# Kernel optimization log

Measured on AMD Instinct MI355X. Metric: run time of the kernel, lower is better.

The kernel has to match this reference:

```python
import jax, jax.numpy as jnp
import numpy as np

B, C, H, Wd, IN_CAPS = 128, 32, 12, 12, 8
OUT_CH, OUT_CAPS, ROUTING_ITERS = 10, 16, 3


def setup_inputs() -> dict:
    key = jax.random.key(0)
    k1, k2 = jax.random.split(key)
    x = jax.random.normal(k1, (B, C, H, Wd, IN_CAPS), dtype=jnp.float32)
    W = jax.random.normal(k2, (1, 1, C, OUT_CH, OUT_CAPS, IN_CAPS), dtype=jnp.float32)
    return {"x": x, "W": W}


def _squash(s):
    # s: [..., out_caps]
    sn = jnp.sum(s * s, axis=-1, keepdims=True)
    return sn * s / ((1.0 + sn) * jnp.sqrt(sn))


def reference(x, W):
    b = x.shape[0]
    # [B, H, W, C, in_caps]
    u = jnp.transpose(x, (0, 2, 3, 1, 4))
    Wm = W[0, 0]  # [C, out_ch, out_caps, in_caps]
    # u_hat[b,h,w,c,o,p] = sum_q Wm[c,o,p,q] * u[b,h,w,c,q]
    u_hat = jnp.einsum('copq,bhwcq->bhwcop', Wm, u)
    u_hat = u_hat.reshape(b, -1, OUT_CH, OUT_CAPS)  # [B, N, O, P]

    b_ij = jnp.zeros(u_hat.shape[:-1], dtype=u_hat.dtype)  # [B, N, O]
    v_j = None
    for i in range(ROUTING_ITERS):
        c_ij = jax.nn.softmax(b_ij, axis=-1)[..., None]  # [B, N, O, 1]
        s_j = jnp.sum(c_ij * u_hat, axis=1)              # [B, O, P]
        v_j = _squash(s_j)                               # [B, O, P]
        if i < ROUTING_ITERS - 1:
            a_j = jnp.sum(u_hat * v_j[:, None], axis=-1)  # [B, N, O]
            b_ij = b_ij + a_j
    return v_j
```

## Files before the change

### kernel.cpp

```cpp
#include <hip/hip_runtime.h>


#define BB 128
#define CC 32
#define HWN 144
#define QQ 8
#define OO 10
#define PP 16

__global__ __launch_bounds__(256, 1)
void digitcaps_routing(const float* __restrict__ x, const float* __restrict__ Wm,
                       float* __restrict__ out) {
    const int b    = blockIdx.x;
    const int tid  = threadIdx.x;
    const int c    = tid >> 3;
    const int slot = tid & 7;

    __shared__ float usum_s[CC * QQ];
    __shared__ float Wv_s[CC * OO * QQ];
    __shared__ float t_s[CC * OO * QQ];
    __shared__ float v_s[OO * PP];

    const float* xb = x + (size_t)b * (CC * HWN * QQ);
    const float* xc = xb + c * (HWN * QQ);

    float us[QQ];
#pragma unroll
    for (int q = 0; q < QQ; ++q) us[q] = 0.f;
#pragma unroll
    for (int i = 0; i < 18; ++i) {
        const int hw = slot + (i << 3);
        const float4* p4 = (const float4*)(xc + hw * QQ);
        float4 a = p4[0], d = p4[1];
        us[0] += a.x; us[1] += a.y; us[2] += a.z; us[3] += a.w;
        us[4] += d.x; us[5] += d.y; us[6] += d.z; us[7] += d.w;
    }
#pragma unroll
    for (int m = 1; m <= 4; m <<= 1) {
#pragma unroll
        for (int q = 0; q < QQ; ++q) us[q] += __shfl_xor(us[q], m);
    }
    if (slot == 0) {
#pragma unroll
        for (int q = 0; q < QQ; ++q) usum_s[c * QQ + q] = us[q];
    }
    __syncthreads();

    if (tid < OO * PP) {
        const int o = tid >> 4, p = tid & 15;
        float s = 0.f;
        for (int cc = 0; cc < CC; ++cc) {
            const float4* w4 = (const float4*)(Wm + (((cc * OO + o) * PP + p) * QQ));
            float4 w0 = w4[0], w1 = w4[1];
            const float* u0 = &usum_s[cc * QQ];
            s += w0.x * u0[0] + w0.y * u0[1] + w0.z * u0[2] + w0.w * u0[3]
               + w1.x * u0[4] + w1.y * u0[5] + w1.z * u0[6] + w1.w * u0[7];
        }
        s *= 0.1f;
        float sn = s * s;
#pragma unroll
        for (int m = 1; m <= 8; m <<= 1) sn += __shfl_xor(sn, m);
        const float fac = sqrtf(sn) / (1.f + sn);
        v_s[tid] = s * fac;
    }
    for (int k = tid; k < CC * OO * QQ; k += 256) Wv_s[k] = 0.f;
    __syncthreads();

    for (int iter = 0; iter < 2; ++iter) {
        for (int k = tid; k < CC * OO * QQ; k += 256) {
            const int cc  = k / (OO * QQ);
            const int rem = k - cc * (OO * QQ);
            const int o   = rem >> 3, q = rem & 7;
            const float* wp = Wm + ((cc * OO + o) * PP) * QQ + q;
            float acc = 0.f;
#pragma unroll
            for (int p = 0; p < PP; ++p) acc += wp[p * QQ] * v_s[o * PP + p];
            Wv_s[k] += acc;
        }
        __syncthreads();

        float wv[OO][QQ];
#pragma unroll
        for (int o = 0; o < OO; ++o)
#pragma unroll
            for (int q = 0; q < QQ; ++q) wv[o][q] = Wv_s[(c * OO + o) * QQ + q];

        float tl[OO][QQ];
#pragma unroll
        for (int o = 0; o < OO; ++o)
#pragma unroll
            for (int q = 0; q < QQ; ++q) tl[o][q] = 0.f;

        for (int i = 0; i < 18; ++i) {
            const int hw = slot + (i << 3);
            const float4* p4 = (const float4*)(xc + hw * QQ);
            float4 a = p4[0], d = p4[1];
            float u[QQ] = {a.x, a.y, a.z, a.w, d.x, d.y, d.z, d.w};
            float lg[OO];
            float mx = -1e30f;
#pragma unroll
            for (int o = 0; o < OO; ++o) {
                float t = 0.f;
#pragma unroll
                for (int q = 0; q < QQ; ++q) t += u[q] * wv[o][q];
                lg[o] = t;
                mx = fmaxf(mx, t);
            }
            float ssum = 0.f;
#pragma unroll
            for (int o = 0; o < OO; ++o) { lg[o] = __expf(lg[o] - mx); ssum += lg[o]; }
            const float inv = 1.f / ssum;
#pragma unroll
            for (int o = 0; o < OO; ++o) {
                const float cij = lg[o] * inv;
#pragma unroll
                for (int q = 0; q < QQ; ++q) tl[o][q] += cij * u[q];
            }
        }
#pragma unroll
        for (int m = 1; m <= 4; m <<= 1) {
#pragma unroll
            for (int o = 0; o < OO; ++o)
#pragma unroll
                for (int q = 0; q < QQ; ++q) tl[o][q] += __shfl_xor(tl[o][q], m);
        }
        if (slot == 0) {
#pragma unroll
            for (int o = 0; o < OO; ++o)
#pragma unroll
                for (int q = 0; q < QQ; ++q) t_s[(c * OO + o) * QQ + q] = tl[o][q];
        }
        __syncthreads();

        if (tid < OO * PP) {
            const int o = tid >> 4, p = tid & 15;
            float s = 0.f;
            for (int cc = 0; cc < CC; ++cc) {
                const float4* w4 = (const float4*)(Wm + (((cc * OO + o) * PP + p) * QQ));
                float4 w0 = w4[0], w1 = w4[1];
                const float* t0 = &t_s[(cc * OO + o) * QQ];
                s += w0.x * t0[0] + w0.y * t0[1] + w0.z * t0[2] + w0.w * t0[3]
                   + w1.x * t0[4] + w1.y * t0[5] + w1.z * t0[6] + w1.w * t0[7];
            }
            float sn = s * s;
#pragma unroll
            for (int m = 1; m <= 8; m <<= 1) sn += __shfl_xor(sn, m);
            const float fac = sqrtf(sn) / (1.f + sn);
            const float v = s * fac;
            if (iter == 1) out[(size_t)b * (OO * PP) + tid] = v;
            else           v_s[tid] = v;
        }
        __syncthreads();
    }
}

extern "C" void kernel_launch(void* const* d_in, const int* in_sizes, int n_in,
                              void* d_out, int out_size, void* d_ws, size_t ws_size,
                              hipStream_t stream) {
    const float* x  = (const float*)d_in[0];
    const float* Wm = (const float*)d_in[1];
    float* out = (float*)d_out;
    digitcaps_routing<<<BB, 256, 0, stream>>>(x, Wm, out);
}
```

Measured before the change: 104.5 us.

## Split routing into multi-kernel pipeline with per-(batch,channel) blocks

Replaces the single 128-block fused routing kernel with six launches: a per-(batch,channel) input sum, a per-batch squash kernel, and a per-(batch,channel) softmax-weighted accumulation kernel run twice. This spreads work over 4096 blocks so many more compute units are busy, where before only 128 blocks ran. The cost is extra launch overhead, intermediate results round-tripping through global workspace, re-reading x per iteration, and a shared-memory transpose reduction in place of shuffles.

```diff
diff --git a/kernel.cpp b/kernel.cpp
--- a/kernel.cpp
+++ b/kernel.cpp
@@ -1,156 +1,136 @@
 #include <hip/hip_runtime.h>
 
 
-#define BB 128
 #define CC 32
 #define HWN 144
 #define QQ 8
 #define OO 10
 #define PP 16
+#define EE 80
 
-__global__ __launch_bounds__(256, 1)
-void digitcaps_routing(const float* __restrict__ x, const float* __restrict__ Wm,
-                       float* __restrict__ out) {
-    const int b    = blockIdx.x;
-    const int tid  = threadIdx.x;
-    const int c    = tid >> 3;
-    const int slot = tid & 7;
-
-    __shared__ float usum_s[CC * QQ];
-    __shared__ float Wv_s[CC * OO * QQ];
-    __shared__ float t_s[CC * OO * QQ];
-    __shared__ float v_s[OO * PP];
-
-    const float* xb = x + (size_t)b * (CC * HWN * QQ);
-    const float* xc = xb + c * (HWN * QQ);
+__global__ __launch_bounds__(64)
+void k_pre(const float* __restrict__ x, float* __restrict__ t) {
+    const int blk = blockIdx.x;
+    const int l   = threadIdx.x;
+    const float* xc = x + (size_t)blk * (HWN * QQ);
 
     float us[QQ];
 #pragma unroll
     for (int q = 0; q < QQ; ++q) us[q] = 0.f;
-#pragma unroll
-    for (int i = 0; i < 18; ++i) {
-        const int hw = slot + (i << 3);
+    for (int hw = l; hw < HWN; hw += 64) {
         const float4* p4 = (const float4*)(xc + hw * QQ);
         float4 a = p4[0], d = p4[1];
         us[0] += a.x; us[1] += a.y; us[2] += a.z; us[3] += a.w;
         us[4] += d.x; us[5] += d.y; us[6] += d.z; us[7] += d.w;
     }
 #pragma unroll
-    for (int m = 1; m <= 4; m <<= 1) {
+    for (int m = 1; m <= 32; m <<= 1) {
 #pragma unroll
         for (int q = 0; q < QQ; ++q) us[q] += __shfl_xor(us[q], m);
     }
-    if (slot == 0) {
+    float* tb = t + (size_t)blk * EE;
+    tb[l] = 0.1f * us[l & 7];
+    if (l < 16) tb[64 + l] = 0.1f * us[l & 7];
+}
+
+__global__ __launch_bounds__(192)
+void k_v(const float* __restrict__ Wm, const float* __restrict__ t,
+         float* __restrict__ v) {
+    const int b = blockIdx.x, tid = threadIdx.x;
+    if (tid >= OO * PP) return;
+    const int o = tid >> 4, p = tid & 15;
+    float s = 0.f;
+    for (int cc = 0; cc < CC; ++cc) {
+        const float4* w4 = (const float4*)(Wm + (((cc * OO + o) * PP + p) * QQ));
+        const float4* t4 = (const float4*)(t + ((size_t)(b * CC + cc)) * EE + o * QQ);
+        float4 w0 = w4[0], w1 = w4[1];
+        float4 t0 = t4[0], t1 = t4[1];
+        s += w0.x * t0.x + w0.y * t0.y + w0.z * t0.z + w0.w * t0.w
+           + w1.x * t1.x + w1.y * t1.y + w1.z * t1.z + w1.w * t1.w;
+    }
+    float sn = s * s;
 #pragma unroll
-        for (int q = 0; q < QQ; ++q) usum_s[c * QQ + q] = us[q];
+    for (int m = 1; m <= 8; m <<= 1) sn += __shfl_xor(sn, m);
+    const float fac = sqrtf(sn) / (1.f + sn);
+    v[b * (OO * PP) + tid] = s * fac;
+}
+
+__global__ __launch_bounds__(64)
+void k_t(const float* __restrict__ x, const float* __restrict__ Wm,
+         const float* __restrict__ v1, const float* __restrict__ v2, int nv,
+         float* __restrict__ t) {
+    const int blk = blockIdx.x;
+    const int b = blk >> 5, c = blk & 31;
+    const int l = threadIdx.x;
+
+    __shared__ float v_s[OO * PP];
+    __shared__ float wv_s[EE];
+    __shared__ float tl_s[64][EE];
+
+    for (int e = l; e < OO * PP; e += 64) {
+        float vv = v1[b * (OO * PP) + e];
+        if (nv == 2) vv += v2[b * (OO * PP) + e];
+        v_s[e] = vv;
     }
     __syncthreads();
 
-    if (tid < OO * PP) {
-        const int o = tid >> 4, p = tid & 15;
-        float s = 0.f;
-        for (int cc = 0; cc < CC; ++cc) {
-            const float4* w4 = (const float4*)(Wm + (((cc * OO + o) * PP + p) * QQ));
-            float4 w0 = w4[0], w1 = w4[1];
-            const float* u0 = &usum_s[cc * QQ];
-            s += w0.x * u0[0] + w0.y * u0[1] + w0.z * u0[2] + w0.w * u0[3]
-               + w1.x * u0[4] + w1.y * u0[5] + w1.z * u0[6] + w1.w * u0[7];
-        }
-        s *= 0.1f;
-        float sn = s * s;
+    for (int e = l; e < EE; e += 64) {
+        const int o = e >> 3, q = e & 7;
+        const float* wp = Wm + ((size_t)(c * OO + o) * PP) * QQ + q;
+        float acc = 0.f;
 #pragma unroll
-        for (int m = 1; m <= 8; m <<= 1) sn += __shfl_xor(sn, m);
-        const float fac = sqrtf(sn) / (1.f + sn);
-        v_s[tid] = s * fac;
+        for (int p = 0; p < PP; ++p) acc += wp[p * QQ] * v_s[o * PP + p];
+        wv_s[e] = acc;
     }
-    for (int k = tid; k < CC * OO * QQ; k += 256) Wv_s[k] = 0.f;
     __syncthreads();
 
-    for (int iter = 0; iter < 2; ++iter) {
-        for (int k = tid; k < CC * OO * QQ; k += 256) {
-            const int cc  = k / (OO * QQ);
-            const int rem = k - cc * (OO * QQ);
-            const int o   = rem >> 3, q = rem & 7;
-            const float* wp = Wm + ((cc * OO + o) * PP) * QQ + q;
-            float acc = 0.f;
+    float wv[EE];
 #pragma unroll
-            for (int p = 0; p < PP; ++p) acc += wp[p * QQ] * v_s[o * PP + p];
-            Wv_s[k] += acc;
+    for (int e = 0; e < EE; ++e) wv[e] = wv_s[e];
+
+    float tl[EE];
+#pragma unroll
+    for (int e = 0; e < EE; ++e) tl[e] = 0.f;
+
+    const float* xc = x + (size_t)blk * (HWN * QQ);
+    for (int hw = l; hw < HWN; hw += 64) {
+        const float4* p4 = (const float4*)(xc + hw * QQ);
+        float4 a = p4[0], d = p4[1];
+        float u[QQ] = {a.x, a.y, a.z, a.w, d.x, d.y, d.z, d.w};
+        float lg[OO];
+        float mx = -1e30f;
+#pragma unroll
+        for (int o = 0; o < OO; ++o) {
+            float s = 0.f;
+#pragma unroll
+            for (int q = 0; q < QQ; ++q) s += u[q] * wv[o * QQ + q];
+            lg[o] = s;
+            mx = fmaxf(mx, s);
         }
-        __syncthreads();
+        float ssum = 0.f;
+#pragma unroll
+        for (int o = 0; o < OO; ++o) { lg[o] = __expf(lg[o] - mx); ssum += lg[o]; }
+        const float inv = 1.f / ssum;
+#pragma unroll
+        for (int o = 0; o < OO; ++o) {
+            const float cij = lg[o] * inv;
+#pragma unroll
+            for (int q = 0; q < QQ; ++q) tl[o * QQ + q] += cij * u[q];
+        }
+    }
 
-        float wv[OO][QQ];
 #pragma unroll
-        for (int o = 0; o < OO; ++o)
-#pragma unroll
-            for (int q = 0; q < QQ; ++q) wv[o][q] = Wv_s[(c * OO + o) * QQ + q];
+    for (int e = 0; e < EE; ++e) tl_s[l][e] = tl[e];
+    __syncthreads();
 
-        float tl[OO][QQ];
-#pragma unroll
-        for (int o = 0; o < OO; ++o)
-#pragma unroll
-            for (int q = 0; q < QQ; ++q) tl[o][q] = 0.f;
-
-        for (int i = 0; i < 18; ++i) {
-            const int hw = slot + (i << 3);
-            const float4* p4 = (const float4*)(xc + hw * QQ);
-            float4 a = p4[0], d = p4[1];
-            float u[QQ] = {a.x, a.y, a.z, a.w, d.x, d.y, d.z, d.w};
-            float lg[OO];
-            float mx = -1e30f;
-#pragma unroll
-            for (int o = 0; o < OO; ++o) {
-                float t = 0.f;
-#pragma unroll
-                for (int q = 0; q < QQ; ++q) t += u[q] * wv[o][q];
-                lg[o] = t;
-                mx = fmaxf(mx, t);
-            }
-            float ssum = 0.f;
-#pragma unroll
-            for (int o = 0; o < OO; ++o) { lg[o] = __expf(lg[o] - mx); ssum += lg[o]; }
-            const float inv = 1.f / ssum;
-#pragma unroll
-            for (int o = 0; o < OO; ++o) {
-                const float cij = lg[o] * inv;
-#pragma unroll
-                for (int q = 0; q < QQ; ++q) tl[o][q] += cij * u[q];
-            }
-        }
-#pragma unroll
-        for (int m = 1; m <= 4; m <<= 1) {
-#pragma unroll
-            for (int o = 0; o < OO; ++o)
-#pragma unroll
-                for (int q = 0; q < QQ; ++q) tl[o][q] += __shfl_xor(tl[o][q], m);
-        }
-        if (slot == 0) {
-#pragma unroll
-            for (int o = 0; o < OO; ++o)
-#pragma unroll
-                for (int q = 0; q < QQ; ++q) t_s[(c * OO + o) * QQ + q] = tl[o][q];
-        }
-        __syncthreads();
-
-        if (tid < OO * PP) {
-            const int o = tid >> 4, p = tid & 15;
-            float s = 0.f;
-            for (int cc = 0; cc < CC; ++cc) {
-                const float4* w4 = (const float4*)(Wm + (((cc * OO + o) * PP + p) * QQ));
-                float4 w0 = w4[0], w1 = w4[1];
-                const float* t0 = &t_s[(cc * OO + o) * QQ];
-                s += w0.x * t0[0] + w0.y * t0[1] + w0.z * t0[2] + w0.w * t0[3]
-                   + w1.x * t0[4] + w1.y * t0[5] + w1.z * t0[6] + w1.w * t0[7];
-            }
-            float sn = s * s;
-#pragma unroll
-            for (int m = 1; m <= 8; m <<= 1) sn += __shfl_xor(sn, m);
-            const float fac = sqrtf(sn) / (1.f + sn);
-            const float v = s * fac;
-            if (iter == 1) out[(size_t)b * (OO * PP) + tid] = v;
-            else           v_s[tid] = v;
-        }
-        __syncthreads();
+    float acc0 = 0.f;
+    for (int j = 0; j < 64; ++j) acc0 += tl_s[(j + l) & 63][l];
+    float* tb = t + (size_t)blk * EE;
+    tb[l] = acc0;
+    if (l < 16) {
+        float acc1 = 0.f;
+        for (int j = 0; j < 64; ++j) acc1 += tl_s[(j + l) & 63][l + 64];
+        tb[64 + l] = acc1;
     }
 }
 
@@ -160,5 +140,15 @@
     const float* x  = (const float*)d_in[0];
     const float* Wm = (const float*)d_in[1];
     float* out = (float*)d_out;
-    digitcaps_routing<<<BB, 256, 0, stream>>>(x, Wm, out);
+
+    float* t  = (float*)d_ws;
+    float* v1 = t + 4096 * EE;
+    float* v2 = v1 + 128 * OO * PP;
+
+    k_pre<<<4096, 64, 0, stream>>>(x, t);
+    k_v  <<<128, 192, 0, stream>>>(Wm, t, v1);
+    k_t  <<<4096, 64, 0, stream>>>(x, Wm, v1, v1, 1, t);
+    k_v  <<<128, 192, 0, stream>>>(Wm, t, v2);
+    k_t  <<<4096, 64, 0, stream>>>(x, Wm, v1, v2, 2, t);
+    k_v  <<<128, 192, 0, stream>>>(Wm, t, out);
 }
```

Measured after the change: 131.1 us. 1.25x slower.
